# Kernel optimization log

Measured on AMD Instinct MI355X. Metric: run time of the kernel, lower is better.

## Reference

```python
import jax, jax.numpy as jnp
import numpy as np

GROUP, BS, CH = 16, 8192, 256


def setup_inputs() -> dict:
    key = jax.random.key(0)
    kx, kw = jax.random.split(key)
    x = jax.random.normal(kx, (GROUP, BS, CH), dtype=jnp.float32)
    # PyTorch init: uniform(-stdv, stdv), stdv = 1/sqrt(channels)
    stdv = 1.0 / np.sqrt(CH)
    weight = jax.random.uniform(kw, (GROUP, CH, CH), dtype=jnp.float32,
                                minval=-stdv, maxval=stdv)
    return {"x": x, "weight": weight}


def reference(x, weight):
    # x: (group, bs, n); weight: (group, n, channels). For each column i of
    # weight (w: (group, n)) apply Householder-style reflection sequentially:
    #   x <- x - (2 / (w^T w)) * (x @ w) w^T
    ws = jnp.moveaxis(weight, -1, 0)  # (channels, group, n)

    def step(xc, w):
        denom = jnp.sum(w * w, axis=-1)              # (group,)
        xw = jnp.einsum('gbn,gn->gb', xc, w)         # (group, bs)
        xc = xc - (2.0 / denom)[:, None, None] * xw[..., None] * w[:, None, :]
        return xc, None

    out, _ = jax.lax.scan(step, x, ws)
    return out
```

## Files before the change

kernel.cpp:

```cpp
#include <hip/hip_runtime.h>
#include <hip/hip_bf16.h>

#define GROUPS 16
#define BSZ    8192
#define CHN    256

using f32x4  = __attribute__((ext_vector_type(4))) float;
using bf16x8 = __attribute__((ext_vector_type(8))) __bf16;

static __device__ __forceinline__ unsigned short f32_bf16(float f) {
    unsigned int u = __builtin_bit_cast(unsigned int, f);
    u = (u + 0x7FFFu + ((u >> 16) & 1u)) >> 16;
    return (unsigned short)u;
}
static __device__ __forceinline__ unsigned int pack_bf16x2(float lo, float hi) {
    return (unsigned int)f32_bf16(lo) | ((unsigned int)f32_bf16(hi) << 16);
}
static __device__ __forceinline__ bf16x8 pack8(float4 u, float4 v) {
    uint4 d;
    d.x = pack_bf16x2(u.x, u.y);
    d.y = pack_bf16x2(u.z, u.w);
    d.z = pack_bf16x2(v.x, v.y);
    d.w = pack_bf16x2(v.z, v.w);
    return __builtin_bit_cast(bf16x8, d);
}

__global__ __launch_bounds__(256) void compose_m(const float* __restrict__ weight,
                                                 unsigned short* __restrict__ Mt) {
    __shared__ float wbuf[16 * 260];
    __shared__ float coefbuf[16];

    const int t    = threadIdx.x;
    const int g    = blockIdx.x >> 4;
    const int r0   = (blockIdx.x & 15) * 16;
    const int lane = t & 15;
    const int rg   = (t >> 4) & 3;
    const int wave = t >> 6;
    const int r    = r0 + wave * 4 + rg;

    float4 m4[4];
#pragma unroll
    for (int j = 0; j < 4; ++j) {
        const int cb = 4 * lane + 64 * j;
        m4[j].x = (cb + 0 == r) ? 1.0f : 0.0f;
        m4[j].y = (cb + 1 == r) ? 1.0f : 0.0f;
        m4[j].z = (cb + 2 == r) ? 1.0f : 0.0f;
        m4[j].w = (cb + 3 == r) ? 1.0f : 0.0f;
    }

    const float* wg = weight + (size_t)g * CHN * CHN;
    const int e16 = t & 15;
    const int nb  = t >> 4;

    float ld[16];
#pragma unroll
    for (int k = 0; k < 16; ++k)
        ld[k] = wg[(nb + 16 * k) * CHN + e16];

    for (int iw = 0; iw < 16; ++iw) {
        __syncthreads();
#pragma unroll
        for (int k = 0; k < 16; ++k)
            wbuf[e16 * 260 + nb + 16 * k] = ld[k];
        __syncthreads();
        if (iw < 15) {
            const int i0 = (iw + 1) * 16;
#pragma unroll
            for (int k = 0; k < 16; ++k)
                ld[k] = wg[(nb + 16 * k) * CHN + i0 + e16];
        }
        {
            const int e = t >> 4;
            float s = 0.0f;
#pragma unroll
            for (int k = 0; k < 16; ++k) {
                const float w = wbuf[e * 260 + lane + 16 * k];
                s += w * w;
            }
            s += __shfl_xor(s, 1);
            s += __shfl_xor(s, 2);
            s += __shfl_xor(s, 4);
            s += __shfl_xor(s, 8);
            if (lane == 0) coefbuf[e] = 2.0f / s;
        }
        __syncthreads();
#pragma unroll
        for (int e = 0; e < 16; ++e) {
            float4 w4[4];
#pragma unroll
            for (int j = 0; j < 4; ++j)
                w4[j] = *(const float4*)&wbuf[e * 260 + 4 * lane + 64 * j];
            float p0 = m4[0].x * w4[0].x + m4[0].y * w4[0].y +
                       m4[0].z * w4[0].z + m4[0].w * w4[0].w;
            float p1 = m4[1].x * w4[1].x + m4[1].y * w4[1].y +
                       m4[1].z * w4[1].z + m4[1].w * w4[1].w;
            float p2 = m4[2].x * w4[2].x + m4[2].y * w4[2].y +
                       m4[2].z * w4[2].z + m4[2].w * w4[2].w;
            float p3 = m4[3].x * w4[3].x + m4[3].y * w4[3].y +
                       m4[3].z * w4[3].z + m4[3].w * w4[3].w;
            float p = (p0 + p1) + (p2 + p3);
            p += __shfl_xor(p, 1);
            p += __shfl_xor(p, 2);
            p += __shfl_xor(p, 4);
            p += __shfl_xor(p, 8);
            const float s = coefbuf[e] * p;
#pragma unroll
            for (int j = 0; j < 4; ++j) {
                m4[j].x -= s * w4[j].x;
                m4[j].y -= s * w4[j].y;
                m4[j].z -= s * w4[j].z;
                m4[j].w -= s * w4[j].w;
            }
        }
    }

    unsigned short* mg = Mt + (size_t)g * CHN * CHN;
#pragma unroll
    for (int j = 0; j < 4; ++j) {
        const int cb = 4 * lane + 64 * j;
        mg[(size_t)(cb + 0) * CHN + r] = f32_bf16(m4[j].x);
        mg[(size_t)(cb + 1) * CHN + r] = f32_bf16(m4[j].y);
        mg[(size_t)(cb + 2) * CHN + r] = f32_bf16(m4[j].z);
        mg[(size_t)(cb + 3) * CHN + r] = f32_bf16(m4[j].w);
    }
}

__global__ __launch_bounds__(256, 2) void gemm_stream(const float* __restrict__ x,
                                                      const unsigned short* __restrict__ Mt,
                                                      float* __restrict__ out) {
    const int t    = threadIdx.x;
    const int wave = t >> 6;
    const int l    = t & 63;
    const int lm   = l & 15;
    const int q    = l >> 4;
    const int g    = blockIdx.x >> 6;
    const int rb   = blockIdx.x & 63;
    const int r0   = rb * 128 + wave * 32;

    const float*          xg = x  + ((size_t)g * BSZ + r0) * CHN;
    const unsigned short* mg = Mt +  (size_t)g * CHN * CHN;

    f32x4 acc[2][16];
#pragma unroll
    for (int mi = 0; mi < 2; ++mi)
#pragma unroll
        for (int ni = 0; ni < 16; ++ni)
            acc[mi][ni] = (f32x4){0.f, 0.f, 0.f, 0.f};

    const float*          xa0 = xg + (size_t)(lm)      * CHN + q * 8;
    const float*          xa1 = xg + (size_t)(16 + lm) * CHN + q * 8;
    const unsigned short* mb  = mg + (size_t)lm * CHN + q * 8;

    for (int kc = 0; kc < 8; ++kc) {
        const int k0 = kc * 32;
        const float4 a00 = *(const float4*)(xa0 + k0);
        const float4 a01 = *(const float4*)(xa0 + k0 + 4);
        const float4 a10 = *(const float4*)(xa1 + k0);
        const float4 a11 = *(const float4*)(xa1 + k0 + 4);
        uint4 bv[16];
#pragma unroll
        for (int ni = 0; ni < 16; ++ni)
            bv[ni] = *(const uint4*)(mb + (size_t)ni * 16 * CHN + k0);

        const bf16x8 a0 = pack8(a00, a01);
        const bf16x8 a1 = pack8(a10, a11);
#pragma unroll
        for (int ni = 0; ni < 16; ++ni) {
            const bf16x8 b = __builtin_bit_cast(bf16x8, bv[ni]);
            acc[0][ni] = __builtin_amdgcn_mfma_f32_16x16x32_bf16(a0, b, acc[0][ni], 0, 0, 0);
            acc[1][ni] = __builtin_amdgcn_mfma_f32_16x16x32_bf16(a1, b, acc[1][ni], 0, 0, 0);
        }
    }

    float* og = out + ((size_t)g * BSZ + r0) * CHN;
#pragma unroll
    for (int mi = 0; mi < 2; ++mi) {
#pragma unroll
        for (int ni = 0; ni < 16; ++ni) {
            const int col = ni * 16 + lm;
#pragma unroll
            for (int reg = 0; reg < 4; ++reg) {
                const int row = mi * 16 + q * 4 + reg;
                og[(size_t)row * CHN + col] = acc[mi][ni][reg];
            }
        }
    }
}

extern "C" void kernel_launch(void* const* d_in, const int* in_sizes, int n_in,
                              void* d_out, int out_size, void* d_ws, size_t ws_size,
                              hipStream_t stream) {
    const float* x = (const float*)d_in[0];
    const float* w = (const float*)d_in[1];
    float* out = (float*)d_out;
    unsigned short* Mt = (unsigned short*)d_ws;

    hipLaunchKernelGGL(compose_m,   dim3(GROUPS * 16), dim3(256), 0, stream, w, Mt);
    hipLaunchKernelGGL(gemm_stream, dim3(GROUPS * 64), dim3(256), 0, stream, x, Mt, out);
}
```

Baseline: 353.1 us.

## Stage half of composed matrix in LDS and split GEMM by column halves

Replaces the streaming GEMM with a kernel where each 512-thread block loads a 128-column half of the bf16 composed matrix into padded shared memory once, then loops over 512 rows of x. X fragments are software-prefetched one k-chunk ahead. The goal is to stop re-reading the matrix from global/L2 per wave and to cut register pressure so more waves fit per CU. The trade-off is that each x row is now read twice, once per column half, and shared-memory reads use scalar dword loads.

```diff
diff --git a/kernel.cpp b/kernel.cpp
--- a/kernel.cpp
+++ b/kernel.cpp
@@ -4,6 +4,8 @@
 #define GROUPS 16
 #define BSZ    8192
 #define CHN    256
+#define COLH   128
+#define BSTR   133
 
 using f32x4  = __attribute__((ext_vector_type(4))) float;
 using bf16x8 = __attribute__((ext_vector_type(8))) __bf16;
@@ -125,65 +127,71 @@
     }
 }
 
-__global__ __launch_bounds__(256, 2) void gemm_stream(const float* __restrict__ x,
-                                                      const unsigned short* __restrict__ Mt,
-                                                      float* __restrict__ out) {
-    const int t    = threadIdx.x;
-    const int wave = t >> 6;
-    const int l    = t & 63;
-    const int lm   = l & 15;
-    const int q    = l >> 4;
-    const int g    = blockIdx.x >> 6;
-    const int rb   = blockIdx.x & 63;
-    const int r0   = rb * 128 + wave * 32;
-
-    const float*          xg = x  + ((size_t)g * BSZ + r0) * CHN;
-    const unsigned short* mg = Mt +  (size_t)g * CHN * CHN;
-
-    f32x4 acc[2][16];
-#pragma unroll
-    for (int mi = 0; mi < 2; ++mi)
-#pragma unroll
-        for (int ni = 0; ni < 16; ++ni)
-            acc[mi][ni] = (f32x4){0.f, 0.f, 0.f, 0.f};
-
-    const float*          xa0 = xg + (size_t)(lm)      * CHN + q * 8;
-    const float*          xa1 = xg + (size_t)(16 + lm) * CHN + q * 8;
-    const unsigned short* mb  = mg + (size_t)lm * CHN + q * 8;
-
-    for (int kc = 0; kc < 8; ++kc) {
-        const int k0 = kc * 32;
-        const float4 a00 = *(const float4*)(xa0 + k0);
-        const float4 a01 = *(const float4*)(xa0 + k0 + 4);
-        const float4 a10 = *(const float4*)(xa1 + k0);
-        const float4 a11 = *(const float4*)(xa1 + k0 + 4);
-        uint4 bv[16];
-#pragma unroll
-        for (int ni = 0; ni < 16; ++ni)
-            bv[ni] = *(const uint4*)(mb + (size_t)ni * 16 * CHN + k0);
-
-        const bf16x8 a0 = pack8(a00, a01);
-        const bf16x8 a1 = pack8(a10, a11);
-#pragma unroll
-        for (int ni = 0; ni < 16; ++ni) {
-            const bf16x8 b = __builtin_bit_cast(bf16x8, bv[ni]);
-            acc[0][ni] = __builtin_amdgcn_mfma_f32_16x16x32_bf16(a0, b, acc[0][ni], 0, 0, 0);
-            acc[1][ni] = __builtin_amdgcn_mfma_f32_16x16x32_bf16(a1, b, acc[1][ni], 0, 0, 0);
-        }
-    }
-
-    float* og = out + ((size_t)g * BSZ + r0) * CHN;
-#pragma unroll
-    for (int mi = 0; mi < 2; ++mi) {
-#pragma unroll
-        for (int ni = 0; ni < 16; ++ni) {
-            const int col = ni * 16 + lm;
-#pragma unroll
-            for (int reg = 0; reg < 4; ++reg) {
-                const int row = mi * 16 + q * 4 + reg;
-                og[(size_t)row * CHN + col] = acc[mi][ni][reg];
+__global__ __launch_bounds__(512, 4) void gemm_bcol(const float* __restrict__ x,
+                                                    const unsigned short* __restrict__ Mt,
+                                                    float* __restrict__ out) {
+    __shared__ unsigned int bsh[COLH * BSTR];
+
+    const int t        = threadIdx.x;
+    const int chalf    = blockIdx.x & 1;
+    const int rowchunk = (blockIdx.x >> 1) & 15;
+    const int g        = blockIdx.x >> 5;
+
+    {
+        const int col = t >> 2;
+        const int kq  = t & 3;
+        const uint4* src = (const uint4*)(Mt + ((size_t)g * CHN + chalf * COLH + col) * CHN);
+#pragma unroll
+        for (int s = 0; s < 8; ++s) {
+            const uint4 v = src[kq * 8 + s];
+            unsigned int* d = &bsh[col * BSTR + (kq * 8 + s) * 4];
+            d[0] = v.x; d[1] = v.y; d[2] = v.z; d[3] = v.w;
+        }
+    }
+    __syncthreads();
+
+    const int w  = t >> 6;
+    const int l  = t & 63;
+    const int lm = l & 15;
+    const int q  = l >> 4;
+
+    const float* xg = x   + (size_t)g * BSZ * CHN;
+    float*       og = out + (size_t)g * BSZ * CHN;
+
+    for (int s = 0; s < 4; ++s) {
+        const int row0 = rowchunk * 512 + s * 128 + w * 16;
+        const float* xp = xg + (size_t)(row0 + lm) * CHN + q * 8;
+
+        f32x4 acc[8];
+#pragma unroll
+        for (int ni = 0; ni < 8; ++ni)
+            acc[ni] = (f32x4){0.f, 0.f, 0.f, 0.f};
+
+        float4 c0 = *(const float4*)(xp);
+        float4 c1 = *(const float4*)(xp + 4);
+#pragma unroll
+        for (int kc = 0; kc < 8; ++kc) {
+            const int kn = (kc < 7) ? kc + 1 : kc;
+            const float4 n0 = *(const float4*)(xp + kn * 32);
+            const float4 n1 = *(const float4*)(xp + kn * 32 + 4);
+            const bf16x8 a = pack8(c0, c1);
+#pragma unroll
+            for (int ni = 0; ni < 8; ++ni) {
+                const unsigned int* bp = &bsh[(ni * 16 + lm) * BSTR + kc * 16 + q * 4];
+                uint4 u;
+                u.x = bp[0]; u.y = bp[1]; u.z = bp[2]; u.w = bp[3];
+                acc[ni] = __builtin_amdgcn_mfma_f32_16x16x32_bf16(
+                    a, __builtin_bit_cast(bf16x8, u), acc[ni], 0, 0, 0);
             }
-        }
+            c0 = n0; c1 = n1;
+        }
+
+        float* ob = og + (size_t)(row0 + q * 4) * CHN + chalf * COLH + lm;
+#pragma unroll
+        for (int ni = 0; ni < 8; ++ni)
+#pragma unroll
+            for (int reg = 0; reg < 4; ++reg)
+                ob[(size_t)reg * CHN + ni * 16] = acc[ni][reg];
     }
 }
 
@@ -195,6 +203,6 @@
     float* out = (float*)d_out;
     unsigned short* Mt = (unsigned short*)d_ws;
 
-    hipLaunchKernelGGL(compose_m,   dim3(GROUPS * 16), dim3(256), 0, stream, w, Mt);
-    hipLaunchKernelGGL(gemm_stream, dim3(GROUPS * 64), dim3(256), 0, stream, x, Mt, out);
-}
+    hipLaunchKernelGGL(compose_m, dim3(GROUPS * 16),     dim3(256), 0, stream, w, Mt);
+    hipLaunchKernelGGL(gemm_bcol, dim3(GROUPS * 16 * 2), dim3(512), 0, stream, x, Mt, out);
+}
```

Result: slower. 501.7 us (+42.1%).
